# Kernel optimization log

Measured on AMD Instinct MI355X. Metric: run time of the kernel, lower is better.

Reference implementation:

```python
import jax, jax.numpy as jnp
import numpy as np

B, M, D = 2048, 40, 64          # batch, num fields, embedding dim
HIDDEN = [128, 128, 128]        # CIN layer sizes


def setup_inputs() -> dict:
    key = jax.random.key(0)
    kx, k0, k1, k2 = jax.random.split(key, 4)
    x = jax.random.normal(kx, (B, M, D), dtype=jnp.float32)
    # torch.rand -> uniform [0, 1)
    W0 = jax.random.uniform(k0, (M, M, HIDDEN[0]), dtype=jnp.float32)
    W1 = jax.random.uniform(k1, (M, HIDDEN[0], HIDDEN[1]), dtype=jnp.float32)
    W2 = jax.random.uniform(k2, (M, HIDDEN[1], HIDDEN[2]), dtype=jnp.float32)
    return {"x": x, "W0": W0, "W1": W1, "W2": W2}


def _cin_forward(x, Ws):
    # x: [b, m, d]. Each layer k:
    #   x_next[b, l, d] = sum_{m, h} x0[b, m, d] * x_k[b, h, d] * W_k[m, h, l]
    # which equals the torch 'bil,bjl->bjil' outer product followed by
    # 'bijk,ijl->bkl' + transpose, but expressed as one fused contraction
    # (opt_einsum picks a path avoiding the worst intermediate).
    ps = []
    xk = x  # [b, H_k, d], H_0 = m
    for W in Ws:
        x_next = jnp.einsum('bmd,bhd,mhl->bld', x, xk, W)  # [b, L_k, d]
        ps.append(jnp.sum(x_next, axis=2))                  # [b, L_k]
        xk = x_next
    return jnp.concatenate(ps, axis=1)                      # [b, sum(L_k)]


def reference(x, W0, W1, W2):
    return _cin_forward(x, (W0, W1, W2))
```

## Files before the change

### kernel.cpp

```cpp
#include <hip/hip_runtime.h>
#include <hip/hip_bf16.h>
#include <cstdint>

#define BATCH 2048
#define MF    40
#define DDIM  64
#define LDIM  128
#define ROWS  (BATCH * DDIM)

typedef __attribute__((ext_vector_type(4)))  short   short4_t;
typedef __attribute__((ext_vector_type(8)))  short   short8;
typedef __attribute__((ext_vector_type(8)))  __bf16  bf16x8;
typedef __attribute__((ext_vector_type(4)))  float   floatx4;
typedef __attribute__((ext_vector_type(16))) float   floatx16;

__device__ __forceinline__ unsigned short f32_to_bf16(float f) {
    union { float f; uint32_t u; } v; v.f = f;
    uint32_t u = v.u;
    uint32_t r = (u + 0x7fffu + ((u >> 16) & 1u)) >> 16;
    return (unsigned short)r;
}

__global__ void k_wprep(const float* __restrict__ W, unsigned short* __restrict__ Wt,
                        int KK, int H) {
    int bi = blockIdx.x;
    int lane = threadIdx.x;
    int cb = bi & 3;
    int mkk = bi >> 2;
    int kk = mkk % KK, m = mkk / KK;
    int l = cb * 32 + (lane & 31);
    int hbase = kk * 16 + (lane >> 5) * 8;
    unsigned short o[8];
#pragma unroll
    for (int j = 0; j < 8; ++j) {
        int h = hbase + j;
        float v = (h < H) ? W[((size_t)m * H + h) * LDIM + l] : 0.f;
        o[j] = f32_to_bf16(v);
    }
    *(short8*)(Wt + ((size_t)bi * 64 + lane) * 8) = *(const short8*)o;
}

template <int KK, bool FIRST, int OFF, bool WRITEX>
__global__ __launch_bounds__(256, 2) void k_gemm(
    const float* __restrict__ x,
    const unsigned short* __restrict__ Xprev,
    const unsigned short* __restrict__ Wt,
    unsigned short* __restrict__ Xout,
    float* __restrict__ out)
{
    __shared__ unsigned short slab[2][KK * 2048];

    const int tid  = threadIdx.x;
    const int lane = tid & 63, wave = tid >> 6;
    const int hf   = lane >> 5, r31 = lane & 31;
    const int rowhalf = wave >> 1, colhalf = wave & 1;
    const int b = blockIdx.x * 2 + rowhalf;

    bf16x8 afrag[2][KK];
    if constexpr (FIRST) {
#pragma unroll
        for (int t = 0; t < 2; ++t)
#pragma unroll
            for (int kk = 0; kk < KK; ++kk) {
                unsigned short tmp[8];
#pragma unroll
                for (int j = 0; j < 8; ++j) {
                    int h = kk * 16 + hf * 8 + j;
                    float v = (h < MF) ? x[((size_t)b * MF + h) * DDIM + t * 32 + r31] : 0.f;
                    tmp[j] = f32_to_bf16(v);
                }
                afrag[t][kk] = __builtin_bit_cast(bf16x8, *(const short8*)tmp);
            }
    } else {
        const int g = r31 >> 3, hs = (r31 >> 2) & 1, ii = r31 & 3;
#pragma unroll
        for (int t = 0; t < 2; ++t) {
            int tile = b * 2 + t;
#pragma unroll
            for (int kk = 0; kk < KK; ++kk) {
                int k0  = kk * 16 + hf * 8;
                int cbk = k0 >> 5, rr = k0 & 31;
                const unsigned short* p =
                    Xprev + ((size_t)(((tile * 4 + cbk) * 4 + g) * 2 + hs) * 32 + rr) * 4 + ii;
                unsigned short tmp[8];
#pragma unroll
                for (int j = 0; j < 8; ++j) tmp[j] = p[(size_t)j * 4];
                afrag[t][kk] = __builtin_bit_cast(bf16x8, *(const short8*)tmp);
            }
        }
    }

    floatx16 acc[2][2] = {};

    auto stage = [&](int m, int buf) {
        const unsigned short* src = Wt + (size_t)m * (KK * 2048);
#pragma unroll
        for (int it = 0; it < KK; ++it) {
            int c = it * 256 + tid;
            __builtin_amdgcn_global_load_lds(
                (const __attribute__((address_space(1))) uint32_t*)(src + (size_t)c * 8),
                (__attribute__((address_space(3))) uint32_t*)(&slab[buf][(size_t)c * 8]),
                16, 0, 0);
        }
    };

    stage(0, 0);
#pragma unroll 1
    for (int m = 0; m < MF; ++m) {
        asm volatile("s_waitcnt vmcnt(0)" ::: "memory");
        __syncthreads();
        if (m + 1 < MF) stage(m + 1, (m + 1) & 1);

        const unsigned short* sl = slab[m & 1];
        const floatx4* sp4 = (const floatx4*)(x + ((size_t)b * MF + m) * DDIM);

#pragma unroll
        for (int cbp = 0; cbp < 2; ++cbp) {
            const int cbg = colhalf * 2 + cbp;
            floatx16 P0{}, P1{};
#pragma unroll
            for (int kk = 0; kk < KK; ++kk) {
                bf16x8 bf = __builtin_bit_cast(
                    bf16x8, *(const short8*)(sl + ((size_t)(kk * 4 + cbg) * 64 + lane) * 8));
                P0 = __builtin_amdgcn_mfma_f32_32x32x16_bf16(afrag[0][kk], bf, P0, 0, 0, 0);
                P1 = __builtin_amdgcn_mfma_f32_32x32x16_bf16(afrag[1][kk], bf, P1, 0, 0, 0);
            }
#pragma unroll
            for (int g = 0; g < 4; ++g) {
                floatx4 s0 = sp4[hf + 2 * g];
                floatx4 s1 = sp4[8 + hf + 2 * g];
#pragma unroll
                for (int i = 0; i < 4; ++i) {
                    acc[0][cbp][g * 4 + i] += s0[i] * P0[g * 4 + i];
                    acc[1][cbp][g * 4 + i] += s1[i] * P1[g * 4 + i];
                }
            }
        }
    }

    if constexpr (WRITEX) {
#pragma unroll
        for (int t = 0; t < 2; ++t) {
            int tile = b * 2 + t;
#pragma unroll
            for (int cbp = 0; cbp < 2; ++cbp) {
                int cb = colhalf * 2 + cbp;
#pragma unroll
                for (int g = 0; g < 4; ++g) {
                    unsigned short o[4];
#pragma unroll
                    for (int i = 0; i < 4; ++i) o[i] = f32_to_bf16(acc[t][cbp][g * 4 + i]);
                    *(short4_t*)(Xout +
                        ((size_t)(((tile * 4 + cb) * 4 + g) * 2 + hf) * 32 + r31) * 4) =
                        *(const short4_t*)o;
                }
            }
        }
    }

#pragma unroll
    for (int cbp = 0; cbp < 2; ++cbp) {
        float v = 0.f;
#pragma unroll
        for (int j = 0; j < 16; ++j) v += acc[0][cbp][j] + acc[1][cbp][j];
        v += __shfl_xor(v, 32);
        if (hf == 0)
            out[(size_t)b * 384 + OFF + (colhalf * 2 + cbp) * 32 + r31] = v;
    }
}

extern "C" void kernel_launch(void* const* d_in, const int* in_sizes, int n_in,
                              void* d_out, int out_size, void* d_ws, size_t ws_size,
                              hipStream_t stream) {
    const float* x  = (const float*)d_in[0];
    const float* W0 = (const float*)d_in[1];
    const float* W1 = (const float*)d_in[2];
    const float* W2 = (const float*)d_in[3];
    float* out = (float*)d_out;

    char* ws = (char*)d_ws;
    size_t off = 0;
    auto alloc = [&](size_t bytes) -> void* {
        void* p = ws + off;
        off += (bytes + 255) & ~(size_t)255;
        return p;
    };
    unsigned short* W0t = (unsigned short*)alloc((size_t)MF * 3 * 2048 * 2);
    unsigned short* W1t = (unsigned short*)alloc((size_t)MF * 8 * 2048 * 2);
    unsigned short* W2t = (unsigned short*)alloc((size_t)MF * 8 * 2048 * 2);
    unsigned short* X1p = (unsigned short*)alloc((size_t)ROWS * LDIM * 2);
    unsigned short* X2p = (unsigned short*)alloc((size_t)ROWS * LDIM * 2);

    k_wprep<<<MF * 3 * 4, 64, 0, stream>>>(W0, W0t, 3, 40);
    k_wprep<<<MF * 8 * 4, 64, 0, stream>>>(W1, W1t, 8, 128);
    k_wprep<<<MF * 8 * 4, 64, 0, stream>>>(W2, W2t, 8, 128);

    k_gemm<3, true,  0,   true ><<<ROWS / 128, 256, 0, stream>>>(x, nullptr, W0t, X1p, out);
    k_gemm<8, false, 128, true ><<<ROWS / 128, 256, 0, stream>>>(x, X1p,     W1t, X2p, out);
    k_gemm<8, false, 256, false><<<ROWS / 128, 256, 0, stream>>>(x, X2p,     W2t, X2p, out);
}
```

Measured before the change: 491.5 us.

## Pre-scale A fragments by x0 and accumulate directly in MFMA, register-prefetch weights

Instead of computing per-m partial products P and then scaling them by x0[b,m,d] on the vector ALUs, the A fragments (indexed by d along rows) are multiplied by the scalar x0 value before the MFMA. This lets the MFMA accumulate straight into the final accumulators and removes the extra FMA epilogue per m. The LDS double-buffered weight staging is replaced by direct global loads into a small register ring buffer with prefetch distance D. The scaled operands are re-rounded to bf16, which adds rounding error, and weight reuse across waves now goes through cache rather than LDS.

```diff
diff --git a/kernel.cpp b/kernel.cpp
--- a/kernel.cpp
+++ b/kernel.cpp
@@ -8,17 +8,34 @@
 #define LDIM  128
 #define ROWS  (BATCH * DDIM)
 
-typedef __attribute__((ext_vector_type(4)))  short   short4_t;
-typedef __attribute__((ext_vector_type(8)))  short   short8;
-typedef __attribute__((ext_vector_type(8)))  __bf16  bf16x8;
-typedef __attribute__((ext_vector_type(4)))  float   floatx4;
-typedef __attribute__((ext_vector_type(16))) float   floatx16;
+typedef __attribute__((ext_vector_type(4)))  short    short4_t;
+typedef __attribute__((ext_vector_type(8)))  short    short8;
+typedef __attribute__((ext_vector_type(8)))  __bf16   bf16x8;
+typedef __attribute__((ext_vector_type(4)))  float    floatx4;
+typedef __attribute__((ext_vector_type(16))) float    floatx16;
+typedef __attribute__((ext_vector_type(4)))  uint32_t uint4_t;
 
 __device__ __forceinline__ unsigned short f32_to_bf16(float f) {
     union { float f; uint32_t u; } v; v.f = f;
     uint32_t u = v.u;
     uint32_t r = (u + 0x7fffu + ((u >> 16) & 1u)) >> 16;
     return (unsigned short)r;
+}
+
+__device__ __forceinline__ uint32_t scale2(uint32_t w, float s) {
+    float lo = __builtin_bit_cast(float, w << 16);
+    float hi = __builtin_bit_cast(float, w & 0xffff0000u);
+    uint32_t plo = __builtin_bit_cast(uint32_t, lo * s) + 0x8000u;
+    uint32_t phi = __builtin_bit_cast(uint32_t, hi * s) + 0x8000u;
+    return __builtin_amdgcn_perm(phi, plo, 0x07060302u);
+}
+
+__device__ __forceinline__ bf16x8 scale_frag(bf16x8 a, float s) {
+    uint4_t w = __builtin_bit_cast(uint4_t, a);
+    uint4_t r;
+#pragma unroll
+    for (int i = 0; i < 4; ++i) r[i] = scale2(w[i], s);
+    return __builtin_bit_cast(bf16x8, r);
 }
 
 __global__ void k_wprep(const float* __restrict__ W, unsigned short* __restrict__ Wt,
@@ -48,8 +65,6 @@
     unsigned short* __restrict__ Xout,
     float* __restrict__ out)
 {
-    __shared__ unsigned short slab[2][KK * 2048];
-
     const int tid  = threadIdx.x;
     const int lane = tid & 63, wave = tid >> 6;
     const int hf   = lane >> 5, r31 = lane & 31;
@@ -92,50 +107,44 @@
 
     floatx16 acc[2][2] = {};
 
-    auto stage = [&](int m, int buf) {
-        const unsigned short* src = Wt + (size_t)m * (KK * 2048);
-#pragma unroll
-        for (int it = 0; it < KK; ++it) {
-            int c = it * 256 + tid;
-            __builtin_amdgcn_global_load_lds(
-                (const __attribute__((address_space(1))) uint32_t*)(src + (size_t)c * 8),
-                (__attribute__((address_space(3))) uint32_t*)(&slab[buf][(size_t)c * 8]),
-                16, 0, 0);
-        }
+    const int cbg0 = colhalf * 2, cbg1 = colhalf * 2 + 1;
+    auto ldg = [&](int flat, int cb) {
+        return __builtin_bit_cast(
+            bf16x8, *(const short8*)(Wt + (((size_t)flat * 4 + cb) * 64 + lane) * 8));
     };
 
-    stage(0, 0);
+    constexpr int NST = MF * KK;
+    constexpr int D = (KK % 4 == 0) ? 4 : KK;
+
+    bf16x8 bbuf[D][2];
+#pragma unroll
+    for (int p = 0; p < D; ++p) { bbuf[p][0] = ldg(p, cbg0); bbuf[p][1] = ldg(p, cbg1); }
+
+    const float* sb = x + (size_t)b * MF * DDIM + r31;
+    float s0 = sb[0], s1 = sb[32];
+    float sn0, sn1;
+
 #pragma unroll 1
     for (int m = 0; m < MF; ++m) {
-        asm volatile("s_waitcnt vmcnt(0)" ::: "memory");
         __syncthreads();
-        if (m + 1 < MF) stage(m + 1, (m + 1) & 1);
-
-        const unsigned short* sl = slab[m & 1];
-        const floatx4* sp4 = (const floatx4*)(x + ((size_t)b * MF + m) * DDIM);
-
-#pragma unroll
-        for (int cbp = 0; cbp < 2; ++cbp) {
-            const int cbg = colhalf * 2 + cbp;
-            floatx16 P0{}, P1{};
-#pragma unroll
-            for (int kk = 0; kk < KK; ++kk) {
-                bf16x8 bf = __builtin_bit_cast(
-                    bf16x8, *(const short8*)(sl + ((size_t)(kk * 4 + cbg) * 64 + lane) * 8));
-                P0 = __builtin_amdgcn_mfma_f32_32x32x16_bf16(afrag[0][kk], bf, P0, 0, 0, 0);
-                P1 = __builtin_amdgcn_mfma_f32_32x32x16_bf16(afrag[1][kk], bf, P1, 0, 0, 0);
-            }
-#pragma unroll
-            for (int g = 0; g < 4; ++g) {
-                floatx4 s0 = sp4[hf + 2 * g];
-                floatx4 s1 = sp4[8 + hf + 2 * g];
-#pragma unroll
-                for (int i = 0; i < 4; ++i) {
-                    acc[0][cbp][g * 4 + i] += s0[i] * P0[g * 4 + i];
-                    acc[1][cbp][g * 4 + i] += s1[i] * P1[g * 4 + i];
-                }
-            }
+        int mn = (m + 1 < MF) ? m + 1 : m;
+        sn0 = sb[(size_t)mn * DDIM];
+        sn1 = sb[(size_t)mn * DDIM + 32];
+#pragma unroll
+        for (int kk = 0; kk < KK; ++kk) {
+            const int slot = kk % D;
+            bf16x8 z0 = scale_frag(afrag[0][kk], s0);
+            bf16x8 z1 = scale_frag(afrag[1][kk], s1);
+            acc[0][0] = __builtin_amdgcn_mfma_f32_32x32x16_bf16(z0, bbuf[slot][0], acc[0][0], 0, 0, 0);
+            acc[0][1] = __builtin_amdgcn_mfma_f32_32x32x16_bf16(z0, bbuf[slot][1], acc[0][1], 0, 0, 0);
+            acc[1][0] = __builtin_amdgcn_mfma_f32_32x32x16_bf16(z1, bbuf[slot][0], acc[1][0], 0, 0, 0);
+            acc[1][1] = __builtin_amdgcn_mfma_f32_32x32x16_bf16(z1, bbuf[slot][1], acc[1][1], 0, 0, 0);
+            int pf = m * KK + kk + D;
+            if (pf > NST - 1) pf = NST - 1;
+            bbuf[slot][0] = ldg(pf, cbg0);
+            bbuf[slot][1] = ldg(pf, cbg1);
         }
+        s0 = sn0; s1 = sn1;
     }
 
     if constexpr (WRITEX) {
```

After: 528.4 us. 7.5% more time.
